# Kernel optimization log

Hardware: AMD Instinct MI355X
Metric: run time of the kernel (lower is better)

Reference implementation:

```python
import jax, jax.numpy as jnp
import numpy as np

N = 100_000   # nodes
E = 1_600_000 # edges
D = 64        # in = hidden = out channels
EPS = 1e-8


def setup_inputs() -> dict:
    key = jax.random.key(0)
    ks = jax.random.split(key, 6)
    s = 1.0 / np.sqrt(D)
    return {
        "x": jax.random.normal(ks[0], (N, D), jnp.float32),
        "edge_index": jax.random.randint(ks[1], (2, E), 0, N, dtype=jnp.int32),
        "W0": jax.random.normal(ks[2], (D, D), jnp.float32) * s,
        "b0": jnp.zeros((D,), jnp.float32),
        "Wm": jax.random.normal(ks[3], (D, D), jnp.float32) * s,
        "bm": jnp.zeros((D,), jnp.float32),
        "W1": jax.random.normal(ks[4], (D, D), jnp.float32) * s,
        "b1": jnp.zeros((D,), jnp.float32),
    }


def _proj_normalize(y):
    # projective (hyperbolic) renormalization onto the unit sphere in R^D
    return y / (jnp.linalg.norm(y, axis=-1, keepdims=True) + EPS)


def _hyp_linear(x, W, b):
    return _proj_normalize(x @ W + b)


def _hinner(u, v):
    # UHG (hyperbolic) bilinear form: <u,v> = u_1..d-1 . v_1..d-1 - u_d * v_d
    return jnp.sum(u[..., :-1] * v[..., :-1], axis=-1) - u[..., -1] * v[..., -1]


def _cross_ratio(x):
    a, b, c, d = x[0], x[1], x[2], x[3]
    return (_hinner(a, c) * _hinner(b, d)) / (_hinner(a, d) * _hinner(b, c) + EPS)


def _maybe_restore_cr(x, cr_init):
    # restore_cross_ratio: rescale x so the 4-point cross-ratio matches cr_init,
    # applied only when the torch guard conditions hold (finite, non-degenerate).
    cr_cur = _cross_ratio(x[:4])
    ratio = cr_init / (cr_cur + EPS)
    cond = ((~jnp.isnan(cr_cur)) & (~jnp.isnan(cr_init))
            & (jnp.abs(cr_cur) > EPS) & (jnp.abs(cr_init) > EPS)
            & (ratio > EPS))
    scale = jnp.where(cond, jnp.sqrt(jnp.abs(ratio)), 1.0)
    x_r = x * scale
    ok = jnp.all(jnp.isfinite(x_r))
    return jnp.where(cond & ok, x_r, x)


def _message_passing(x, src, dst, Wm, bm):
    # gather -> mean-aggregate(scatter) -> hyperbolic linear, preserving cross-ratio
    cr0 = _cross_ratio(x[:4])
    msgs = x[src]                                                  # [E, D] gather
    summed = jax.ops.segment_sum(msgs, dst, num_segments=N)        # [N, D] scatter-add
    cnt = jax.ops.segment_sum(jnp.ones((E,), x.dtype), dst, num_segments=N)
    agg = summed / jnp.maximum(cnt, 1.0)[:, None]                  # mean aggregation
    h = _proj_normalize(agg @ Wm + bm)
    return _maybe_restore_cr(h, cr0)


def reference(x, edge_index, W0, b0, Wm, bm, W1, b1):
    src, dst = edge_index[0], edge_index[1]
    cr_init = _cross_ratio(x[:4])          # N > 3 so has_cr is always True
    h = _hyp_linear(x, W0, b0)             # layers[0]
    # num_layers = 2 -> single message-passing round (i = 1)
    h = _message_passing(h, src, dst, Wm, bm)
    h = _hyp_linear(h, W1, b1)             # layers[1]
    h = jax.nn.relu(h)                      # act
    h = _maybe_restore_cr(h, cr_init)
    return h
```

## Files before the change

### kernel.cpp

```cpp
#include <hip/hip_runtime.h>
#include <math.h>

#define NNODES 100000
#define NEDGES 1600000
#define DD 64
#define EPS 1e-8f

#define NBUCK 1024
#define BW 98
#define BIN_BLOCKS 256
#define BIN_CHUNK ((NEDGES + BIN_BLOCKS - 1) / BIN_BLOCKS)
#define BIN_CAP 16
#define SORT_CAP 4096
#define NTILES (NNODES / 16)
#define CAP4 512
#define TSTR 68

typedef unsigned short us8 __attribute__((ext_vector_type(8)));
typedef short short8 __attribute__((ext_vector_type(8)));
typedef float f32x4 __attribute__((ext_vector_type(4)));

__device__ __forceinline__ float wave_sum(float v) {
    #pragma unroll
    for (int off = 32; off; off >>= 1) v += __shfl_xor(v, off, 64);
    return v;
}

__device__ __forceinline__ float hinner(float u, float v, float sgn) {
    return wave_sum(sgn * u * v);
}

__device__ __forceinline__ float cross_ratio(float r0, float r1, float r2, float r3, float sgn) {
    float A = hinner(r0, r2, sgn);
    float B = hinner(r1, r3, sgn);
    float C = hinner(r0, r3, sgn);
    float Dv = hinner(r1, r2, sgn);
    return (A * B) / (C * Dv + EPS);
}

__device__ __forceinline__ float restore_scale(float cr_i, float cr_c) {
    float ratio = cr_i / (cr_c + EPS);
    bool cond = (!__builtin_isnan(cr_c)) && (!__builtin_isnan(cr_i)) &&
                (fabsf(cr_c) > EPS) && (fabsf(cr_i) > EPS) && (ratio > EPS);
    float s = 1.0f;
    if (cond) {
        s = sqrtf(fabsf(ratio));
        if (!__builtin_isfinite(s)) s = 1.0f;
    }
    return s;
}

__device__ __forceinline__ unsigned short f2bf(float f) {
    unsigned u = __float_as_uint(f);
    unsigned r = (u + 0x7fffu + ((u >> 16) & 1u)) >> 16;
    return (unsigned short)r;
}

__device__ __forceinline__ float bf2f(unsigned short b) {
    return __uint_as_float(((unsigned)b) << 16);
}

__device__ __forceinline__ float bcast(float v, int lane) {
    return __int_as_float(__builtin_amdgcn_readlane(__float_as_int(v), lane));
}

__device__ __forceinline__ void load_bfrags(const float* __restrict__ W, int lane,
                                            short8 bhi[4][2], short8 blo[4][2]) {
    int c = lane & 15, q = lane >> 4;
    #pragma unroll
    for (int t = 0; t < 4; t++)
        #pragma unroll
        for (int h = 0; h < 2; h++) {
            short8 hi8, lo8;
            #pragma unroll
            for (int j = 0; j < 8; j++) {
                float w = W[(h * 32 + q * 8 + j) * DD + t * 16 + c];
                unsigned short hb = f2bf(w);
                float r = w - bf2f(hb);
                hi8[j] = (short)hb;
                lo8[j] = (short)f2bf(r);
            }
            bhi[t][h] = hi8;
            blo[t][h] = lo8;
        }
}

__device__ __forceinline__ void build_a8(const float av[8], short8& hi, short8& lo) {
    short8 h8, l8;
    #pragma unroll
    for (int j = 0; j < 8; j++) {
        unsigned short hb = f2bf(av[j]);
        float r = av[j] - bf2f(hb);
        h8[j] = (short)hb;
        l8[j] = (short)f2bf(r);
    }
    hi = h8;
    lo = l8;
}

__device__ __forceinline__ void build_a(const float* p, short8& hi, short8& lo) {
    float4 f0 = *(const float4*)p;
    float4 f1 = *(const float4*)(p + 4);
    float av[8] = {f0.x, f0.y, f0.z, f0.w, f1.x, f1.y, f1.z, f1.w};
    build_a8(av, hi, lo);
}

#define MFMA3R(cacc, ahi, alo, BH, BL, t, h)                                     \
    cacc = __builtin_amdgcn_mfma_f32_16x16x32_bf16(ahi, BH[t][h], cacc, 0, 0, 0); \
    cacc = __builtin_amdgcn_mfma_f32_16x16x32_bf16(alo, BH[t][h], cacc, 0, 0, 0); \
    cacc = __builtin_amdgcn_mfma_f32_16x16x32_bf16(ahi, BL[t][h], cacc, 0, 0, 0);

__global__ __launch_bounds__(256, 3) void k_l0h(const float* __restrict__ x,
                                                const float* __restrict__ W0,
                                                const float* __restrict__ b0,
                                                unsigned short* __restrict__ h0b,
                                                const int* __restrict__ ei,
                                                int* __restrict__ bhist) {
    __shared__ int h[NBUCK];
    if (blockIdx.x < 512) {
        for (int i = threadIdx.x; i < NBUCK; i += 256) h[i] = 0;
        __syncthreads();
        int tid = blockIdx.x * 256 + threadIdx.x;
        int stride = 512 * 256;
        for (int e = tid; e < NEDGES; e += stride)
            atomicAdd(&h[(unsigned)ei[NEDGES + e] / BW], 1);
        __syncthreads();
        for (int i = threadIdx.x; i < NBUCK; i += 256)
            if (h[i]) atomicAdd(&bhist[i], h[i]);
        return;
    }
    int bid = blockIdx.x - 512;
    int lane = threadIdx.x & 63;
    int c = lane & 15, q = lane >> 4;
    short8 bhi[4][2], blo[4][2];
    load_bfrags(W0, lane, bhi, blo);
    float badd[4];
    #pragma unroll
    for (int t = 0; t < 4; t++) badd[t] = b0[t * 16 + c];
    int wid = (bid * 256 + threadIdx.x) >> 6;
    int nw = (1024 * 256) >> 6;
    for (int tile = wid; tile < NTILES; tile += nw) {
        int R = tile * 16;
        f32x4 cc[4] = {{0, 0, 0, 0}, {0, 0, 0, 0}, {0, 0, 0, 0}, {0, 0, 0, 0}};
        #pragma unroll
        for (int hh = 0; hh < 2; hh++) {
            short8 ahi, alo;
            build_a(x + ((size_t)(R + c) << 6) + hh * 32 + q * 8, ahi, alo);
            #pragma unroll
            for (int t = 0; t < 4; t++) { MFMA3R(cc[t], ahi, alo, bhi, blo, t, hh); }
        }
        float ss[4];
        #pragma unroll
        for (int r = 0; r < 4; r++) {
            #pragma unroll
            for (int t = 0; t < 4; t++) cc[t][r] += badd[t];
            ss[r] = cc[0][r] * cc[0][r] + cc[1][r] * cc[1][r] +
                    cc[2][r] * cc[2][r] + cc[3][r] * cc[3][r];
        }
        #pragma unroll
        for (int off = 1; off <= 8; off <<= 1) {
            #pragma unroll
            for (int r = 0; r < 4; r++) ss[r] += __shfl_xor(ss[r], off, 64);
        }
        #pragma unroll
        for (int r = 0; r < 4; r++) {
            float sc = 1.0f / (sqrtf(ss[r]) + EPS);
            int row = R + q * 4 + r;
            #pragma unroll
            for (int t = 0; t < 4; t++)
                h0b[(size_t)row * DD + t * 16 + c] = f2bf(cc[t][r] * sc);
        }
    }
}

__global__ __launch_bounds__(NBUCK) void k_scan1024(const int* __restrict__ bhist,
                                                    int* __restrict__ bstart,
                                                    int* __restrict__ gcur,
                                                    int* __restrict__ scratch_cur) {
    __shared__ int s[NBUCK];
    int t = threadIdx.x;
    int v = bhist[t];
    s[t] = v;
    __syncthreads();
    for (int off = 1; off < NBUCK; off <<= 1) {
        int u = (t >= off) ? s[t - off] : 0;
        __syncthreads();
        s[t] += u;
        __syncthreads();
    }
    bstart[t] = s[t] - v;
    gcur[t] = s[t] - v;
    if (t == 0) scratch_cur[0] = 0;
}

__global__ __launch_bounds__(256) void k_bin(const int* __restrict__ ei,
                                             int* __restrict__ gcur,
                                             unsigned* __restrict__ colpack,
                                             int* __restrict__ cnt4,
                                             int* __restrict__ list4) {
    __shared__ unsigned stag[NBUCK * BIN_CAP];
    __shared__ int lcnt[NBUCK];
    int t = threadIdx.x;
    for (int i = t; i < NBUCK; i += 256) lcnt[i] = 0;
    __syncthreads();
    int lo = blockIdx.x * BIN_CHUNK;
    int hi = lo + BIN_CHUNK; if (hi > NEDGES) hi = NEDGES;
    for (int e = lo + t; e < hi; e += 256) {
        int d = ei[NEDGES + e];
        int s = ei[e];
        if ((unsigned)d < 4u) {
            int p = atomicAdd(&cnt4[d], 1);
            if (p < CAP4) list4[d * CAP4 + p] = s;
        }
        unsigned b = (unsigned)d / BW;
        unsigned dl = (unsigned)d - b * BW;
        unsigned pk = ((unsigned)s << 8) | dl;
        int slot = atomicAdd(&lcnt[b], 1);
        if (slot < BIN_CAP) {
            stag[b * BIN_CAP + slot] = pk;
        } else {
            colpack[atomicAdd(&gcur[b], 1)] = pk;
        }
    }
    __syncthreads();
    for (int b = t; b < NBUCK; b += 256) {
        int cnt = lcnt[b];
        if (cnt > BIN_CAP) cnt = BIN_CAP;
        if (cnt > 0) {
            int base = atomicAdd(&gcur[b], cnt);
            for (int i = 0; i < cnt; i++)
                colpack[base + i] = stag[b * BIN_CAP + i];
        }
    }
}

__global__ __launch_bounds__(512, 4) void k_sortAggH(const unsigned* __restrict__ colpack,
                                                     const int* __restrict__ bstart,
                                                     const int* __restrict__ bhist,
                                                     const unsigned short* __restrict__ h0b,
                                                     float* __restrict__ agg,
                                                     int* __restrict__ scratch,
                                                     int* __restrict__ scratch_cur,
                                                     const float* __restrict__ x,
                                                     const float* __restrict__ W0,
                                                     const float* __restrict__ b0,
                                                     const int* __restrict__ cnt4,
                                                     const int* __restrict__ list4,
                                                     const float* __restrict__ Wm,
                                                     const float* __restrict__ bm,
                                                     const float* __restrict__ W1,
                                                     const float* __restrict__ b1,
                                                     float* __restrict__ scal) {
    __shared__ int lcol[SORT_CAP];
    __shared__ int cnt[BW];
    __shared__ int pre[BW];
    __shared__ int sbs;
    int t = threadIdx.x;
    if (blockIdx.x == 0) {
        float* hs  = (float*)lcol;
        float* h2s = hs + 4 * DD;
        float* frs = h2s + 4 * DD;
        int lane = t & 63;
        int w = t >> 6;
        float sgn = (lane == 63) ? -1.0f : 1.0f;
        float s1 = 1.0f;
        float cr_init = 0.0f;
        if (w < 4) {
            float w0[DD];
            #pragma unroll
            for (int k = 0; k < DD; k++) w0[k] = W0[k * DD + lane];
            float b0v = b0[lane];
            auto h0row = [&](int r) -> float {
                float xv = x[(size_t)r * DD + lane];
                float acc = b0v;
                #pragma unroll
                for (int k = 0; k < DD; k++)
                    acc = fmaf(bcast(xv, k), w0[k], acc);
                float n = sqrtf(wave_sum(acc * acc));
                return acc / (n + EPS);
            };
            hs[w * DD + lane] = h0row(w);
            int full = cnt4[w];
            int cl = full; if (cl > CAP4) cl = CAP4;
            float sum = 0.0f;
            for (int i = 0; i < cl; i++) sum += h0row(list4[w * CAP4 + i]);
            float av = sum / fmaxf((float)full, 1.0f);
            float acc = bm[lane];
            #pragma unroll
            for (int k = 0; k < DD; k++)
                acc = fmaf(bcast(av, k), Wm[k * DD + lane], acc);
            float n = sqrtf(wave_sum(acc * acc));
            h2s[w * DD + lane] = acc / (n + EPS);
        }
        __syncthreads();
        if (w < 4) {
            cr_init = cross_ratio(x[lane], x[DD + lane], x[2 * DD + lane], x[3 * DD + lane], sgn);
            float cr0 = cross_ratio(hs[lane], hs[DD + lane], hs[2 * DD + lane], hs[3 * DD + lane], sgn);
            float cr_cur = cross_ratio(h2s[lane], h2s[DD + lane], h2s[2 * DD + lane], h2s[3 * DD + lane], sgn);
            s1 = restore_scale(cr0, cr_cur);
            float hv = h2s[w * DD + lane] * s1;
            float acc2 = b1[lane];
            #pragma unroll
            for (int k = 0; k < DD; k++)
                acc2 = fmaf(bcast(hv, k), W1[k * DD + lane], acc2);
            float n = sqrtf(wave_sum(acc2 * acc2));
            frs[w * DD + lane] = fmaxf(acc2 / (n + EPS), 0.0f);
        }
        __syncthreads();
        if (w == 0) {
            float cr2 = cross_ratio(frs[lane], frs[DD + lane], frs[2 * DD + lane], frs[3 * DD + lane], sgn);
            float s2 = restore_scale(cr_init, cr2);
            if (lane == 0) { scal[0] = s1; scal[1] = s2; }
        }
        return;
    }
    int b = blockIdx.x - 1;
    int nlo = b * BW; if (nlo > NNODES) nlo = NNODES;
    int nhi = nlo + BW; if (nhi > NNODES) nhi = NNODES;
    int nodes = nhi - nlo;
    int base = bstart[b];
    int n = bhist[b];
    for (int i = t; i < BW; i += 512) cnt[i] = 0;
    bool inLds = (n <= SORT_CAP);
    if (t == 0) sbs = inLds ? 0 : atomicAdd(scratch_cur, n);
    __syncthreads();
    int sb = sbs;
    for (int i = t; i < n; i += 512)
        atomicAdd(&cnt[colpack[base + i] & 255u], 1);
    __syncthreads();
    if (t < 64) {
        int v0 = cnt[t];
        int inc0 = v0;
        #pragma unroll
        for (int off = 1; off < 64; off <<= 1) {
            int u = __shfl_up(inc0, off, 64);
            if (t >= off) inc0 += u;
        }
        int tot0 = __builtin_amdgcn_readlane(inc0, 63);
        int ex0 = inc0 - v0;
        int i1 = 64 + t;
        int v1 = (i1 < BW) ? cnt[i1] : 0;
        int inc1 = v1;
        #pragma unroll
        for (int off = 1; off < 64; off <<= 1) {
            int u = __shfl_up(inc1, off, 64);
            if (t >= off) inc1 += u;
        }
        int ex1 = inc1 - v1 + tot0;
        pre[t] = ex0;
        cnt[t] = ex0;
        if (i1 < BW) { pre[i1] = ex1; cnt[i1] = ex1; }
    }
    __syncthreads();
    for (int i = t; i < n; i += 512) {
        unsigned pk = colpack[base + i];
        int pos = atomicAdd(&cnt[pk & 255u], 1);
        int v = (int)(pk >> 8);
        if (inLds) lcol[pos] = v;
        else       scratch[sb + pos] = v;
    }
    __syncthreads();
    int wv = t >> 6, lane = t & 63;
    int q = lane & 7, g = lane >> 3;
    auto run_agg = [&](auto ld) {
        for (int dA = wv; dA < nodes; dA += 16) {
            int dB = dA + 8;
            bool hB = dB < nodes;
            int stA = pre[dA], enA = cnt[dA];
            int stB = hB ? pre[dB] : 0, enB = hB ? cnt[dB] : 0;
            int degA = enA - stA, degB = enB - stB;
            int ngA = (degA + 7) >> 3, ngB = (degB + 7) >> 3;
            int ng = ngA > ngB ? ngA : ngB;
            float sA[8] = {0, 0, 0, 0, 0, 0, 0, 0};
            float sB[8] = {0, 0, 0, 0, 0, 0, 0, 0};
            for (int k = 0; k < ng; k++) {
                int eA = stA + k * 8 + g;
                int eB = stB + k * 8 + g;
                bool fA = eA < enA;
                bool fB = eB < enB;
                int iA = ld(fA ? eA : 0);
                int iB = ld(fB ? eB : 0);
                us8 uA = *(const us8*)(h0b + (size_t)iA * DD + q * 8);
                us8 uB = *(const us8*)(h0b + (size_t)iB * DD + q * 8);
                float mA = fA ? 1.0f : 0.0f;
                float mB = fB ? 1.0f : 0.0f;
                #pragma unroll
                for (int i = 0; i < 8; i++) {
                    sA[i] = fmaf(mA, bf2f(uA[i]), sA[i]);
                    sB[i] = fmaf(mB, bf2f(uB[i]), sB[i]);
                }
            }
            #pragma unroll
            for (int i = 0; i < 8; i++) {
                sA[i] += __shfl_xor(sA[i], 8, 64);
                sA[i] += __shfl_xor(sA[i], 16, 64);
                sA[i] += __shfl_xor(sA[i], 32, 64);
                sB[i] += __shfl_xor(sB[i], 8, 64);
                sB[i] += __shfl_xor(sB[i], 16, 64);
                sB[i] += __shfl_xor(sB[i], 32, 64);
            }
            if (g == 0) {
                float invA = 1.0f / fmaxf((float)degA, 1.0f);
                float4* dstA = (float4*)(agg + (size_t)(nlo + dA) * DD + q * 8);
                float4 a0 = {sA[0] * invA, sA[1] * invA, sA[2] * invA, sA[3] * invA};
                float4 a1 = {sA[4] * invA, sA[5] * invA, sA[6] * invA, sA[7] * invA};
                dstA[0] = a0;
                dstA[1] = a1;
                if (hB) {
                    float invB = 1.0f / fmaxf((float)degB, 1.0f);
                    float4* dstB = (float4*)(agg + (size_t)(nlo + dB) * DD + q * 8);
                    float4 b0v = {sB[0] * invB, sB[1] * invB, sB[2] * invB, sB[3] * invB};
                    float4 b1v = {sB[4] * invB, sB[5] * invB, sB[6] * invB, sB[7] * invB};
                    dstB[0] = b0v;
                    dstB[1] = b1v;
                }
            }
        }
    };
    if (inLds) run_agg([&](int e) { return lcol[e]; });
    else       run_agg([&](int e) { return scratch[sb + e]; });
}

__global__ __launch_bounds__(256, 2) void k_gemm2(float* data,
                                                  const float* __restrict__ Wm,
                                                  const float* __restrict__ bm,
                                                  const float* __restrict__ W1,
                                                  const float* __restrict__ b1,
                                                  const float* __restrict__ scal) {
    __shared__ float tsm[4][16 * TSTR];
    int tid = threadIdx.x;
    int wv = tid >> 6, lane = tid & 63;
    int c = lane & 15, q = lane >> 4;
    short8 bhiM[4][2], bloM[4][2], bhi1[4][2], blo1[4][2];
    load_bfrags(Wm, lane, bhiM, bloM);
    load_bfrags(W1, lane, bhi1, blo1);
    float bmv[4], b1v[4];
    #pragma unroll
    for (int t = 0; t < 4; t++) { bmv[t] = bm[t * 16 + c]; b1v[t] = b1[t * 16 + c]; }
    float s1 = scal[0], s2 = scal[1];
    int wid = (blockIdx.x * 256 + tid) >> 6;
    int nw = (gridDim.x * 256) >> 6;
    for (int tile = wid; tile < NTILES; tile += nw) {
        int R = tile * 16;
        f32x4 cc[4] = {{0, 0, 0, 0}, {0, 0, 0, 0}, {0, 0, 0, 0}, {0, 0, 0, 0}};
        #pragma unroll
        for (int hh = 0; hh < 2; hh++) {
            short8 ahi, alo;
            build_a(data + ((size_t)(R + c) << 6) + hh * 32 + q * 8, ahi, alo);
            #pragma unroll
            for (int t = 0; t < 4; t++) { MFMA3R(cc[t], ahi, alo, bhiM, bloM, t, hh); }
        }
        float ss[4];
        #pragma unroll
        for (int r = 0; r < 4; r++) {
            #pragma unroll
            for (int t = 0; t < 4; t++) cc[t][r] += bmv[t];
            ss[r] = cc[0][r] * cc[0][r] + cc[1][r] * cc[1][r] +
                    cc[2][r] * cc[2][r] + cc[3][r] * cc[3][r];
        }
        #pragma unroll
        for (int off = 1; off <= 8; off <<= 1) {
            #pragma unroll
            for (int r = 0; r < 4; r++) ss[r] += __shfl_xor(ss[r], off, 64);
        }
        #pragma unroll
        for (int r = 0; r < 4; r++) {
            float sc = s1 / (sqrtf(ss[r]) + EPS);
            #pragma unroll
            for (int t = 0; t < 4; t++)
                tsm[wv][(q * 4 + r) * TSTR + t * 16 + c] = cc[t][r] * sc;
        }
        f32x4 c2[4] = {{0, 0, 0, 0}, {0, 0, 0, 0}, {0, 0, 0, 0}, {0, 0, 0, 0}};
        #pragma unroll
        for (int hh = 0; hh < 2; hh++) {
            const float* p = &tsm[wv][c * TSTR + hh * 32 + q * 8];
            float av[8];
            #pragma unroll
            for (int j = 0; j < 8; j++) av[j] = p[j];
            short8 ahi, alo;
            build_a8(av, ahi, alo);
            #pragma unroll
            for (int t = 0; t < 4; t++) { MFMA3R(c2[t], ahi, alo, bhi1, blo1, t, hh); }
        }
        #pragma unroll
        for (int r = 0; r < 4; r++) {
            #pragma unroll
            for (int t = 0; t < 4; t++) c2[t][r] += b1v[t];
            ss[r] = c2[0][r] * c2[0][r] + c2[1][r] * c2[1][r] +
                    c2[2][r] * c2[2][r] + c2[3][r] * c2[3][r];
        }
        #pragma unroll
        for (int off = 1; off <= 8; off <<= 1) {
            #pragma unroll
            for (int r = 0; r < 4; r++) ss[r] += __shfl_xor(ss[r], off, 64);
        }
        #pragma unroll
        for (int r = 0; r < 4; r++) {
            float sc = 1.0f / (sqrtf(ss[r]) + EPS);
            int row = R + q * 4 + r;
            #pragma unroll
            for (int t = 0; t < 4; t++)
                data[(size_t)row * DD + t * 16 + c] = fmaxf(c2[t][r] * sc, 0.0f) * s2;
        }
    }
}

extern "C" void kernel_launch(void* const* d_in, const int* in_sizes, int n_in,
                              void* d_out, int out_size, void* d_ws, size_t ws_size,
                              hipStream_t stream) {
    const float* x  = (const float*)d_in[0];
    const int*   ei = (const int*)d_in[1];
    const float* W0 = (const float*)d_in[2];
    const float* b0 = (const float*)d_in[3];
    const float* Wm = (const float*)d_in[4];
    const float* bm = (const float*)d_in[5];
    const float* W1 = (const float*)d_in[6];
    const float* b1 = (const float*)d_in[7];
    float* out = (float*)d_out;

    unsigned short* h0b = (unsigned short*)d_ws;
    int* scratch = (int*)(h0b + (size_t)NNODES * DD);
    unsigned* colpack = (unsigned*)(scratch + NNODES);
    int* bhist  = (int*)(colpack + NEDGES);
    int* cnt4   = bhist + NBUCK;
    int* bstart = cnt4 + 4;
    int* gcur   = bstart + NBUCK;
    int* scur   = gcur + NBUCK;
    int* list4  = scur + 1;
    float* scal = (float*)(list4 + 4 * CAP4);

    (void)hipMemsetAsync(bhist, 0, (NBUCK + 4) * sizeof(int), stream);

    k_l0h     <<<1536, 256, 0, stream>>>(x, W0, b0, h0b, ei, bhist);
    k_scan1024<<<1, NBUCK, 0, stream>>>(bhist, bstart, gcur, scur);
    k_bin     <<<BIN_BLOCKS, 256, 0, stream>>>(ei, gcur, colpack, cnt4, list4);
    k_sortAggH<<<NBUCK, 512, 0, stream>>>(colpack, bstart, bhist, h0b, out, scratch, scur,
                                          x, W0, b0, cnt4, list4, Wm, bm, W1, b1, scal);
    k_gemm2   <<<512, 256, 0, stream>>>(out, Wm, bm, W1, b1, scal);
}
```

Before: 213.2 us.

## Split layer-0 GEMM across histogram and bin kernels; unroll aggregation to four nodes

The layer-0 hyperbolic linear is split into two tile ranges: a small part runs alongside the edge histogram and the rest runs alongside the edge binning kernel. This lets GEMM work hide under the latency-bound atomic passes instead of only the histogram. The mean-aggregation loop now processes four destination nodes per wave iteration instead of two, giving more independent gathers in flight at the cost of more registers. The LDS staging capacity per bucket in binning is reduced, shrinking shared memory so more blocks can be resident but spilling more edges to global atomics.

After: 203.5 us. 1.05x faster.

```diff
diff --git a/kernel.cpp b/kernel.cpp
--- a/kernel.cpp
+++ b/kernel.cpp
@@ -10,9 +10,10 @@
 #define BW 98
 #define BIN_BLOCKS 256
 #define BIN_CHUNK ((NEDGES + BIN_BLOCKS - 1) / BIN_BLOCKS)
-#define BIN_CAP 16
+#define BIN_CAP 12
 #define SORT_CAP 4096
 #define NTILES (NNODES / 16)
+#define TILEA 1250
 #define CAP4 512
 #define TSTR 68
 
@@ -110,36 +111,18 @@
     cacc = __builtin_amdgcn_mfma_f32_16x16x32_bf16(alo, BH[t][h], cacc, 0, 0, 0); \
     cacc = __builtin_amdgcn_mfma_f32_16x16x32_bf16(ahi, BL[t][h], cacc, 0, 0, 0);
 
-__global__ __launch_bounds__(256, 3) void k_l0h(const float* __restrict__ x,
-                                                const float* __restrict__ W0,
-                                                const float* __restrict__ b0,
-                                                unsigned short* __restrict__ h0b,
-                                                const int* __restrict__ ei,
-                                                int* __restrict__ bhist) {
-    __shared__ int h[NBUCK];
-    if (blockIdx.x < 512) {
-        for (int i = threadIdx.x; i < NBUCK; i += 256) h[i] = 0;
-        __syncthreads();
-        int tid = blockIdx.x * 256 + threadIdx.x;
-        int stride = 512 * 256;
-        for (int e = tid; e < NEDGES; e += stride)
-            atomicAdd(&h[(unsigned)ei[NEDGES + e] / BW], 1);
-        __syncthreads();
-        for (int i = threadIdx.x; i < NBUCK; i += 256)
-            if (h[i]) atomicAdd(&bhist[i], h[i]);
-        return;
-    }
-    int bid = blockIdx.x - 512;
-    int lane = threadIdx.x & 63;
+__device__ __forceinline__ void l0_tiles(const float* __restrict__ x,
+                                         const float* __restrict__ W0,
+                                         const float* __restrict__ b0,
+                                         unsigned short* __restrict__ h0b,
+                                         int lane, int wid, int nw, int tlo, int thi) {
     int c = lane & 15, q = lane >> 4;
     short8 bhi[4][2], blo[4][2];
     load_bfrags(W0, lane, bhi, blo);
     float badd[4];
     #pragma unroll
     for (int t = 0; t < 4; t++) badd[t] = b0[t * 16 + c];
-    int wid = (bid * 256 + threadIdx.x) >> 6;
-    int nw = (1024 * 256) >> 6;
-    for (int tile = wid; tile < NTILES; tile += nw) {
+    for (int tile = tlo + wid; tile < thi; tile += nw) {
         int R = tile * 16;
         f32x4 cc[4] = {{0, 0, 0, 0}, {0, 0, 0, 0}, {0, 0, 0, 0}, {0, 0, 0, 0}};
         #pragma unroll
@@ -171,6 +154,30 @@
                 h0b[(size_t)row * DD + t * 16 + c] = f2bf(cc[t][r] * sc);
         }
     }
+}
+
+__global__ __launch_bounds__(256, 3) void k_histoGemmA(const int* __restrict__ ei,
+                                                       int* __restrict__ bhist,
+                                                       const float* __restrict__ x,
+                                                       const float* __restrict__ W0,
+                                                       const float* __restrict__ b0,
+                                                       unsigned short* __restrict__ h0b) {
+    __shared__ int h[NBUCK];
+    if (blockIdx.x < 512) {
+        for (int i = threadIdx.x; i < NBUCK; i += 256) h[i] = 0;
+        __syncthreads();
+        int tid = blockIdx.x * 256 + threadIdx.x;
+        int stride = 512 * 256;
+        for (int e = tid; e < NEDGES; e += stride)
+            atomicAdd(&h[(unsigned)ei[NEDGES + e] / BW], 1);
+        __syncthreads();
+        for (int i = threadIdx.x; i < NBUCK; i += 256)
+            if (h[i]) atomicAdd(&bhist[i], h[i]);
+        return;
+    }
+    int bid = blockIdx.x - 512;
+    int wid = (bid * 256 + threadIdx.x) >> 6;
+    l0_tiles(x, W0, b0, h0b, threadIdx.x & 63, wid, 1024, 0, TILEA);
 }
 
 __global__ __launch_bounds__(NBUCK) void k_scan1024(const int* __restrict__ bhist,
@@ -193,45 +200,55 @@
     if (t == 0) scratch_cur[0] = 0;
 }
 
-__global__ __launch_bounds__(256) void k_bin(const int* __restrict__ ei,
-                                             int* __restrict__ gcur,
-                                             unsigned* __restrict__ colpack,
-                                             int* __restrict__ cnt4,
-                                             int* __restrict__ list4) {
+__global__ __launch_bounds__(256, 3) void k_binGemmB(const float* __restrict__ x,
+                                                     const float* __restrict__ W0,
+                                                     const float* __restrict__ b0,
+                                                     unsigned short* __restrict__ h0b,
+                                                     const int* __restrict__ ei,
+                                                     int* __restrict__ gcur,
+                                                     unsigned* __restrict__ colpack,
+                                                     int* __restrict__ cnt4,
+                                                     int* __restrict__ list4) {
     __shared__ unsigned stag[NBUCK * BIN_CAP];
     __shared__ int lcnt[NBUCK];
     int t = threadIdx.x;
-    for (int i = t; i < NBUCK; i += 256) lcnt[i] = 0;
-    __syncthreads();
-    int lo = blockIdx.x * BIN_CHUNK;
-    int hi = lo + BIN_CHUNK; if (hi > NEDGES) hi = NEDGES;
-    for (int e = lo + t; e < hi; e += 256) {
-        int d = ei[NEDGES + e];
-        int s = ei[e];
-        if ((unsigned)d < 4u) {
-            int p = atomicAdd(&cnt4[d], 1);
-            if (p < CAP4) list4[d * CAP4 + p] = s;
-        }
-        unsigned b = (unsigned)d / BW;
-        unsigned dl = (unsigned)d - b * BW;
-        unsigned pk = ((unsigned)s << 8) | dl;
-        int slot = atomicAdd(&lcnt[b], 1);
-        if (slot < BIN_CAP) {
-            stag[b * BIN_CAP + slot] = pk;
-        } else {
-            colpack[atomicAdd(&gcur[b], 1)] = pk;
-        }
-    }
-    __syncthreads();
-    for (int b = t; b < NBUCK; b += 256) {
-        int cnt = lcnt[b];
-        if (cnt > BIN_CAP) cnt = BIN_CAP;
-        if (cnt > 0) {
-            int base = atomicAdd(&gcur[b], cnt);
-            for (int i = 0; i < cnt; i++)
-                colpack[base + i] = stag[b * BIN_CAP + i];
-        }
-    }
+    if (blockIdx.x < BIN_BLOCKS) {
+        for (int i = t; i < NBUCK; i += 256) lcnt[i] = 0;
+        __syncthreads();
+        int lo = blockIdx.x * BIN_CHUNK;
+        int hi = lo + BIN_CHUNK; if (hi > NEDGES) hi = NEDGES;
+        for (int e = lo + t; e < hi; e += 256) {
+            int d = ei[NEDGES + e];
+            int s = ei[e];
+            if ((unsigned)d < 4u) {
+                int p = atomicAdd(&cnt4[d], 1);
+                if (p < CAP4) list4[d * CAP4 + p] = s;
+            }
+            unsigned b = (unsigned)d / BW;
+            unsigned dl = (unsigned)d - b * BW;
+            unsigned pk = ((unsigned)s << 8) | dl;
+            int slot = atomicAdd(&lcnt[b], 1);
+            if (slot < BIN_CAP) {
+                stag[b * BIN_CAP + slot] = pk;
+            } else {
+                colpack[atomicAdd(&gcur[b], 1)] = pk;
+            }
+        }
+        __syncthreads();
+        for (int b = t; b < NBUCK; b += 256) {
+            int cnt = lcnt[b];
+            if (cnt > BIN_CAP) cnt = BIN_CAP;
+            if (cnt > 0) {
+                int base = atomicAdd(&gcur[b], cnt);
+                for (int i = 0; i < cnt; i++)
+                    colpack[base + i] = stag[b * BIN_CAP + i];
+            }
+        }
+        return;
+    }
+    int bid = blockIdx.x - BIN_BLOCKS;
+    int wid = (bid * 256 + t) >> 6;
+    l0_tiles(x, W0, b0, h0b, t & 63, wid, 4096, TILEA, NTILES);
 }
 
 __global__ __launch_bounds__(512, 4) void k_sortAggH(const unsigned* __restrict__ colpack,
@@ -363,31 +380,46 @@
     int wv = t >> 6, lane = t & 63;
     int q = lane & 7, g = lane >> 3;
     auto run_agg = [&](auto ld) {
-        for (int dA = wv; dA < nodes; dA += 16) {
-            int dB = dA + 8;
-            bool hB = dB < nodes;
+        for (int dA = wv; dA < nodes; dA += 32) {
+            int dB = dA + 8, dC = dA + 16, dD = dA + 24;
+            bool hB = dB < nodes, hC = dC < nodes, hD = dD < nodes;
             int stA = pre[dA], enA = cnt[dA];
             int stB = hB ? pre[dB] : 0, enB = hB ? cnt[dB] : 0;
-            int degA = enA - stA, degB = enB - stB;
-            int ngA = (degA + 7) >> 3, ngB = (degB + 7) >> 3;
+            int stC = hC ? pre[dC] : 0, enC = hC ? cnt[dC] : 0;
+            int stD = hD ? pre[dD] : 0, enD = hD ? cnt[dD] : 0;
+            int ngA = (enA - stA + 7) >> 3, ngB = (enB - stB + 7) >> 3;
+            int ngC = (enC - stC + 7) >> 3, ngD = (enD - stD + 7) >> 3;
             int ng = ngA > ngB ? ngA : ngB;
+            if (ngC > ng) ng = ngC;
+            if (ngD > ng) ng = ngD;
             float sA[8] = {0, 0, 0, 0, 0, 0, 0, 0};
             float sB[8] = {0, 0, 0, 0, 0, 0, 0, 0};
+            float sC[8] = {0, 0, 0, 0, 0, 0, 0, 0};
+            float sD[8] = {0, 0, 0, 0, 0, 0, 0, 0};
             for (int k = 0; k < ng; k++) {
                 int eA = stA + k * 8 + g;
                 int eB = stB + k * 8 + g;
-                bool fA = eA < enA;
-                bool fB = eB < enB;
+                int eC = stC + k * 8 + g;
+                int eD = stD + k * 8 + g;
+                bool fA = eA < enA, fB = eB < enB, fC = eC < enC, fD = eD < enD;
                 int iA = ld(fA ? eA : 0);
                 int iB = ld(fB ? eB : 0);
+                int iC = ld(fC ? eC : 0);
+                int iD = ld(fD ? eD : 0);
                 us8 uA = *(const us8*)(h0b + (size_t)iA * DD + q * 8);
                 us8 uB = *(const us8*)(h0b + (size_t)iB * DD + q * 8);
+                us8 uC = *(const us8*)(h0b + (size_t)iC * DD + q * 8);
+                us8 uD = *(const us8*)(h0b + (size_t)iD * DD + q * 8);
                 float mA = fA ? 1.0f : 0.0f;
                 float mB = fB ? 1.0f : 0.0f;
+                float mC = fC ? 1.0f : 0.0f;
+                float mD = fD ? 1.0f : 0.0f;
                 #pragma unroll
                 for (int i = 0; i < 8; i++) {
                     sA[i] = fmaf(mA, bf2f(uA[i]), sA[i]);
                     sB[i] = fmaf(mB, bf2f(uB[i]), sB[i]);
+                    sC[i] = fmaf(mC, bf2f(uC[i]), sC[i]);
+                    sD[i] = fmaf(mD, bf2f(uD[i]), sD[i]);
                 }
             }
             #pragma unroll
@@ -398,21 +430,43 @@
                 sB[i] += __shfl_xor(sB[i], 8, 64);
                 sB[i] += __shfl_xor(sB[i], 16, 64);
                 sB[i] += __shfl_xor(sB[i], 32, 64);
+                sC[i] += __shfl_xor(sC[i], 8, 64);
+                sC[i] += __shfl_xor(sC[i], 16, 64);
+                sC[i] += __shfl_xor(sC[i], 32, 64);
+                sD[i] += __shfl_xor(sD[i], 8, 64);
+                sD[i] += __shfl_xor(sD[i], 16, 64);
+                sD[i] += __shfl_xor(sD[i], 32, 64);
             }
             if (g == 0) {
-                float invA = 1.0f / fmaxf((float)degA, 1.0f);
+                float invA = 1.0f / fmaxf((float)(enA - stA), 1.0f);
                 float4* dstA = (float4*)(agg + (size_t)(nlo + dA) * DD + q * 8);
                 float4 a0 = {sA[0] * invA, sA[1] * invA, sA[2] * invA, sA[3] * invA};
                 float4 a1 = {sA[4] * invA, sA[5] * invA, sA[6] * invA, sA[7] * invA};
                 dstA[0] = a0;
                 dstA[1] = a1;
                 if (hB) {
-                    float invB = 1.0f / fmaxf((float)degB, 1.0f);
+                    float invB = 1.0f / fmaxf((float)(enB - stB), 1.0f);
                     float4* dstB = (float4*)(agg + (size_t)(nlo + dB) * DD + q * 8);
                     float4 b0v = {sB[0] * invB, sB[1] * invB, sB[2] * invB, sB[3] * invB};
                     float4 b1v = {sB[4] * invB, sB[5] * invB, sB[6] * invB, sB[7] * invB};
                     dstB[0] = b0v;
                     dstB[1] = b1v;
+                }
+                if (hC) {
+                    float invC = 1.0f / fmaxf((float)(enC - stC), 1.0f);
+                    float4* dstC = (float4*)(agg + (size_t)(nlo + dC) * DD + q * 8);
+                    float4 c0 = {sC[0] * invC, sC[1] * invC, sC[2] * invC, sC[3] * invC};
+                    float4 c1 = {sC[4] * invC, sC[5] * invC, sC[6] * invC, sC[7] * invC};
+                    dstC[0] = c0;
+                    dstC[1] = c1;
+                }
+                if (hD) {
+                    float invD = 1.0f / fmaxf((float)(enD - stD), 1.0f);
+                    float4* dstD = (float4*)(agg + (size_t)(nlo + dD) * DD + q * 8);
+                    float4 d0 = {sD[0] * invD, sD[1] * invD, sD[2] * invD, sD[3] * invD};
+                    float4 d1 = {sD[4] * invD, sD[5] * invD, sD[6] * invD, sD[7] * invD};
+                    dstD[0] = d0;
+                    dstD[1] = d1;
                 }
             }
         }
@@ -531,10 +585,10 @@
 
     (void)hipMemsetAsync(bhist, 0, (NBUCK + 4) * sizeof(int), stream);
 
-    k_l0h     <<<1536, 256, 0, stream>>>(x, W0, b0, h0b, ei, bhist);
-    k_scan1024<<<1, NBUCK, 0, stream>>>(bhist, bstart, gcur, scur);
-    k_bin     <<<BIN_BLOCKS, 256, 0, stream>>>(ei, gcur, colpack, cnt4, list4);
-    k_sortAggH<<<NBUCK, 512, 0, stream>>>(colpack, bstart, bhist, h0b, out, scratch, scur,
-                                          x, W0, b0, cnt4, list4, Wm, bm, W1, b1, scal);
-    k_gemm2   <<<512, 256, 0, stream>>>(out, Wm, bm, W1, b1, scal);
-}
+    k_histoGemmA<<<512 + 256, 256, 0, stream>>>(ei, bhist, x, W0, b0, h0b);
+    k_scan1024  <<<1, NBUCK, 0, stream>>>(bhist, bstart, gcur, scur);
+    k_binGemmB  <<<BIN_BLOCKS + 1024, 256, 0, stream>>>(x, W0, b0, h0b, ei, gcur, colpack, cnt4, list4);
+    k_sortAggH  <<<NBUCK, 512, 0, stream>>>(colpack, bstart, bhist, h0b, out, scratch, scur,
+                                            x, W0, b0, cnt4, list4, Wm, bm, W1, b1, scal);
+    k_gemm2     <<<512, 256, 0, stream>>>(out, Wm, bm, W1, b1, scal);
+}
```
